# Performance work log

Measured on AMD Instinct MI355X. Metric: run time of the kernel, lower is better.

Reference implementation:

```python
import jax, jax.numpy as jnp
import numpy as np
from jax import lax

B, S, D, G, V = 32, 8, 128, 32, 64   # batch, slots, hidden_dim, grid_size, vocab_size
K, ED = 128, 32                       # VQ codebook size, code dim


def _conv(x, w, b, pad):
    # standard Conv2d, NCHW / OIHW
    y = lax.conv_general_dilated(x, w, (1, 1), [(pad, pad), (pad, pad)],
                                 dimension_numbers=('NCHW', 'OIHW', 'NCHW'))
    return y + b[None, :, None, None]


def _convT(x, w, b):
    # ConvTranspose2d(k=5, stride=1, padding=2) == conv with spatially flipped
    # kernel, padding k-1-p = 2, channels swapped (IOHW layout of torch weight).
    y = lax.conv_general_dilated(x, jnp.flip(w, (2, 3)), (1, 1), [(2, 2), (2, 2)],
                                 dimension_numbers=('NCHW', 'IOHW', 'NCHW'))
    return y + b[None, :, None, None]


def _build_grid(h, w):
    ys = jnp.linspace(0.0, 1.0, h)
    xs = jnp.linspace(0.0, 1.0, w)
    gy, gx = jnp.meshgrid(ys, xs, indexing='ij')
    g = jnp.stack([gy, gx], axis=-1)                 # [H,W,2]
    return jnp.concatenate([g, 1.0 - g], axis=-1)    # [H,W,4]


def setup_inputs() -> dict:
    key = jax.random.key(0)
    ks = jax.random.split(key, 20)
    sc = 0.05
    n = lambda k, sh: jax.random.normal(k, sh, jnp.float32) * sc
    return {
        'latent': jax.random.normal(ks[0], (B, S, D), jnp.float32),
        'pos_w': n(ks[1], (D, 4)),            # Linear(4, hidden): [out,in]
        'pos_b': jnp.zeros((D,), jnp.float32),
        'ct1_w': n(ks[2], (D, 64, 5, 5)),     # ConvTranspose2d: [in,out,kH,kW]
        'ct1_b': jnp.zeros((64,), jnp.float32),
        'ct2_w': n(ks[3], (64, 32, 5, 5)),
        'ct2_b': jnp.zeros((32,), jnp.float32),
        'codebook': jax.random.uniform(ks[4], (K, ED), jnp.float32, -1.0 / K, 1.0 / K),
        'c1_w': n(ks[5], (64, 32, 3, 3)),     # Conv2d: [out,in,kH,kW]
        'c1_b': jnp.zeros((64,), jnp.float32),
        'c2_w': n(ks[6], (V, 64, 3, 3)),
        'c2_b': jnp.zeros((V,), jnp.float32),
        'a1_w': n(ks[7], (64, 32, 3, 3)),
        'a1_b': jnp.zeros((64,), jnp.float32),
        'a2_w': n(ks[8], (1, 64, 3, 3)),
        'a2_b': jnp.zeros((1,), jnp.float32),
    }


def _forward(latent, pos_w, pos_b, ct1_w, ct1_b, ct2_w, ct2_b, codebook,
             c1_w, c1_b, c2_w, c2_b, a1_w, a1_b, a2_w, a2_b):
    b, s, d = latent.shape
    # spatial broadcast of slot latents -> [B*S, D, H, W]
    z = jnp.broadcast_to(latent.reshape(b * s, d, 1, 1), (b * s, d, G, G))
    # soft position embedding
    grid = _build_grid(G, G)                                  # [H,W,4]
    pos = (grid @ pos_w.T + pos_b).transpose(2, 0, 1)[None]   # [1,D,H,W]
    z = z + pos
    # ConvTranspose decoder
    h = jax.nn.relu(_convT(z, ct1_w, ct1_b))
    feat = jax.nn.relu(_convT(h, ct2_w, ct2_b))               # [B*S,32,H,W]
    # VQ bottleneck on channel-last features
    fp = feat.transpose(0, 2, 3, 1)                           # [B*S,H,W,32]
    flat = fp.reshape(-1, ED)                                 # [N,32]
    dist = (jnp.sum(flat * flat, axis=1, keepdims=True)
            + jnp.sum(codebook * codebook, axis=1)
            - 2.0 * flat @ codebook.T)                        # [N,K]
    idx = jnp.argmin(dist, axis=1)                            # [N]
    q = codebook[idx].reshape(fp.shape)                       # gather lookup
    e_loss = jnp.mean((lax.stop_gradient(q) - fp) ** 2)
    q_loss = jnp.mean((q - lax.stop_gradient(fp)) ** 2)
    vq_loss = q_loss + 0.25 * e_loss
    q_ste = fp + lax.stop_gradient(q - fp)                    # straight-through
    vq_feat = q_ste.transpose(0, 3, 1, 2)                     # [B*S,32,H,W]
    # heads
    colors = _conv(jax.nn.silu(_conv(vq_feat, c1_w, c1_b, 1)), c2_w, c2_b, 1)
    colors = colors.reshape(b, s, V, G, G)
    alphas = _conv(jax.nn.silu(_conv(feat, a1_w, a1_b, 1)), a2_w, a2_b, 1)
    alphas = alphas.reshape(b, s, 1, G, G)
    alphas_n = jax.nn.softmax(alphas, axis=1)
    recon = jnp.sum(alphas_n * colors, axis=1)                # [B,V,H,W]
    return recon, alphas_n, vq_loss


def reference(latent, pos_w, pos_b, ct1_w, ct1_b, ct2_w, ct2_b, codebook,
              c1_w, c1_b, c2_w, c2_b, a1_w, a1_b, a2_w, a2_b):
    return _forward(latent, pos_w, pos_b, ct1_w, ct1_b, ct2_w, ct2_b, codebook,
                    c1_w, c1_b, c2_w, c2_b, a1_w, a1_b, a2_w, a2_b)
```

## Files before the change

kernel.cpp:

```cpp
#include <hip/hip_runtime.h>
#include <math.h>

#define AOFF 2097152
#define LOFF 2359296

typedef __attribute__((ext_vector_type(8))) short short8;
typedef __attribute__((ext_vector_type(4))) float f32x4;

__device__ __forceinline__ int clsf(int v) { return v < 2 ? v : (v > 29 ? v - 27 : 2); }

__device__ __forceinline__ unsigned int f2bfu(float x) {
    unsigned int u = __float_as_uint(x);
    return (u + 0x7FFFu + ((u >> 16) & 1u)) >> 16;
}
__device__ __forceinline__ unsigned int cvt2(float a, float b) {
    return f2bfu(a) | (f2bfu(b) << 16);
}
__device__ __forceinline__ float bf2f(unsigned short u) {
    return __uint_as_float(((unsigned int)u) << 16);
}

__global__ void w1t_kernel(const float* __restrict__ w1, float* __restrict__ w1t) {
    int idx = blockIdx.x * 256 + threadIdx.x;
    if (idx >= 204800) return;
    int tap = idx % 25, rest = idx / 25;
    w1t[tap * 8192 + rest] = w1[idx];
}

__global__ void tapabc_kernel(const float* __restrict__ pw, const float* __restrict__ pb,
                              const float* __restrict__ w1t, float* __restrict__ tapabc) {
    __shared__ float A3[384];
    int tap = blockIdx.x, t = threadIdx.x;
    if (t < 128) {
        float p0 = pw[t * 4], p1 = pw[t * 4 + 1], p2 = pw[t * 4 + 2], p3 = pw[t * 4 + 3];
        A3[t] = p2 + p3 + pb[t];
        A3[128 + t] = p0 - p2;
        A3[256 + t] = p1 - p3;
    }
    __syncthreads();
    int o = t & 63, comp = t >> 6;
    const float* wp = w1t + tap * 8192 + o;
    const float* a = A3 + comp * 128;
    float s = 0.f;
    for (int i = 0; i < 128; ++i) s = fmaf(wp[i * 64], a[i], s);
    tapabc[(tap * 64 + o) * 3 + comp] = s;
}

__global__ void pfill_kernel(const float* __restrict__ tapabc, const float* __restrict__ b1,
                             float* __restrict__ P2) {
    __shared__ float uv[75];
    int o = blockIdx.x, t = threadIdx.x;
    if (t < 75) {
        int cls = t / 3, comp = t % 3;
        int cy = cls / 5, cx = cls % 5;
        const int klo[5] = {2, 1, 0, 0, 0}, khi[5] = {4, 4, 4, 3, 2};
        const float inv31 = 1.f / 31.f;
        float s = (comp == 0) ? b1[o] : 0.f;
        for (int ky = klo[cy]; ky <= khi[cy]; ++ky)
            for (int kx = klo[cx]; kx <= khi[cx]; ++kx) {
                int tap = (4 - ky) * 5 + (4 - kx);
                const float* tp = &tapabc[(tap * 64 + o) * 3];
                if (comp == 0) s += tp[0] + tp[1] * (ky - 2) * inv31 + tp[2] * (kx - 2) * inv31;
                else if (comp == 1) s += tp[1] * inv31;
                else s += tp[2] * inv31;
            }
        uv[t] = s;
    }
    __syncthreads();
    int y = t >> 5, x = t & 31;
    int cls = clsf(y) * 5 + clsf(x);
    float val = uv[cls * 3] + uv[cls * 3 + 1] * y + uv[cls * 3 + 2] * x;
    P2[((o >> 1) << 11) + (t << 1) + (o & 1)] = val;
}

__global__ void wsum_kernel(const float* __restrict__ w1, float* __restrict__ Wsum) {
    int idx = blockIdx.x * 256 + threadIdx.x;
    if (idx >= 25 * 128 * 64) return;
    int cls = idx >> 13;
    int i = (idx >> 6) & 127;
    int o = idx & 63;
    int cy = cls / 5, cx = cls % 5;
    const int klo[5] = {2, 1, 0, 0, 0}, khi[5] = {4, 4, 4, 3, 2};
    float s = 0.f;
    for (int ky = klo[cy]; ky <= khi[cy]; ++ky)
        for (int kx = klo[cx]; kx <= khi[cx]; ++kx)
            s += w1[(i * 64 + o) * 25 + (4 - ky) * 5 + (4 - kx)];
    Wsum[idx] = s;
}

__global__ void m_kernel(const float* __restrict__ latent, const float* __restrict__ Wsum,
                         float* __restrict__ M) {
    int n = blockIdx.x, cls = blockIdx.y, o = threadIdx.x;
    const float* l = &latent[n * 128];
    const float* w = &Wsum[cls * 8192 + o];
    float a0 = 0.f, a1 = 0.f;
    for (int i = 0; i < 128; i += 2) {
        a0 = fmaf(l[i], w[i * 64], a0);
        a1 = fmaf(l[i + 1], w[(i + 1) * 64], a1);
    }
    M[(n * 25 + cls) * 64 + o] = a0 + a1;
}

__global__ void prep_all_kernel(const float* __restrict__ a1w, const float* __restrict__ c1w,
                                const float* __restrict__ c2w, const float* __restrict__ ct2w,
                                short* __restrict__ wtall) {
    int gid = blockIdx.x * 256 + threadIdx.x;
    if (gid < 36864) {
        const float* src = gid < 18432 ? a1w : c1w;
        int idx = gid < 18432 ? gid : gid - 18432;
        int j = idx & 7, fi = idx >> 3;
        int o = fi % 64, g = (fi / 64) & 3, t = fi / 256;
        int i = g * 8 + j;
        wtall[gid] = (short)f2bfu(src[(o * 32 + i) * 9 + (t / 3) * 3 + (t % 3)]);
    } else if (gid < 73728) {
        int idx = gid - 36864;
        int j = idx & 7, fi = idx >> 3;
        int o = fi % 64, g = (fi / 64) & 3, ks = (fi / 256) & 1, t = fi / 512;
        int i = ks * 32 + g * 8 + j;
        wtall[gid] = (short)f2bfu(c2w[(o * 64 + i) * 9 + (t / 3) * 3 + (t % 3)]);
    } else if (gid < 124928) {
        int idx = gid - 73728;
        int j = idx & 7, fi = idx >> 3;
        int o = fi & 31, g = (fi >> 5) & 3, ks = (fi >> 7) & 1, t = fi >> 8;
        int i = ks * 32 + g * 8 + j;
        int ky = t / 5, kx = t % 5;
        wtall[gid] = (short)f2bfu(ct2w[((i * 32 + o) * 5 + (4 - ky)) * 5 + (4 - kx)]);
    }
}

__global__ __launch_bounds__(256, 4) void conv5_kernel(
        const float* __restrict__ M, const float* __restrict__ P2,
        const short* __restrict__ wt, const float* __restrict__ b2,
        unsigned short* __restrict__ featb) {
    __shared__ __align__(16) short tile[12 * 36 * 32];
    __shared__ float Ml[1600];
    const int n = blockIdx.x, y0 = blockIdx.y * 8;
    const int tid = threadIdx.x, w = tid >> 6, l = tid & 63;
    const int lx = l & 15, lg = l >> 4;

    for (int e = tid; e < 1600; e += 256) Ml[e] = M[n * 1600 + e];
    __syncthreads();

    f32x4 acc[2][2][2];
    #pragma unroll
    for (int m = 0; m < 2; ++m)
        #pragma unroll
        for (int q = 0; q < 2; ++q)
            #pragma unroll
            for (int c = 0; c < 2; ++c) acc[m][q][c] = (f32x4){0.f, 0.f, 0.f, 0.f};

    #pragma unroll 1
    for (int ks = 0; ks < 2; ++ks) {
        if (ks) __syncthreads();
        for (int e = tid; e < 6912; e += 256) {
            int cx = e % 36;
            int q = e / 36;
            int ipl = q & 15;
            int r = q >> 4;
            int gy = y0 - 2 + r, gx = cx - 2;
            unsigned int pack = 0u;
            if (gy >= 0 && gy < 32 && gx >= 0 && gx < 32) {
                int cls = clsf(gy) * 5 + clsf(gx);
                int pp = gy * 32 + gx;
                float2 pv = ((const float2*)P2)[((ks * 16 + ipl) << 10) + pp];
                float2 ml = ((const float2*)Ml)[cls * 32 + ks * 16 + ipl];
                pack = cvt2(fmaxf(ml.x + pv.x, 0.f), fmaxf(ml.y + pv.y, 0.f));
            }
            int off = ((r * 36 + cx) * 32 + 2 * ipl) * 2;
            off ^= (cx & 3) << 4;
            *(unsigned int*)((char*)tile + off) = pack;
        }
        __syncthreads();
        #pragma unroll 1
        for (int kx = 0; kx < 5; ++kx) {
            short8 af[5][2];
            #pragma unroll
            for (int ky = 0; ky < 5; ++ky)
                #pragma unroll
                for (int m = 0; m < 2; ++m)
                    af[ky][m] = *(const short8*)(wt + (ky * 5 + kx) * 2048 +
                                                 ((ks * 4 + lg) * 32 + m * 16 + lx) * 8);
            const int key = ((kx + lx) & 3) << 4;
            #pragma unroll
            for (int colf = 0; colf < 2; ++colf) {
                const int cbase = ((2 * w) * 36 + kx + colf * 16 + lx) * 64 + lg * 16;
                short8 bc[6];
                #pragma unroll
                for (int ir = 0; ir < 6; ++ir)
                    bc[ir] = *(const short8*)((char*)tile + ((cbase + ir * (36 * 64)) ^ key));
                #pragma unroll
                for (int ky = 0; ky < 5; ++ky)
                    #pragma unroll
                    for (int q = 0; q < 2; ++q)
                        #pragma unroll
                        for (int m = 0; m < 2; ++m)
                            acc[m][q][colf] = __builtin_amdgcn_mfma_f32_16x16x32_bf16(
                                af[ky][m], bc[q + ky], acc[m][q][colf], 0, 0, 0);
            }
        }
    }

    #pragma unroll
    for (int m = 0; m < 2; ++m)
        #pragma unroll
        for (int q = 0; q < 2; ++q)
            #pragma unroll
            for (int colf = 0; colf < 2; ++colf) {
                int yl = 2 * w + q, x = colf * 16 + lx;
                #pragma unroll
                for (int r = 0; r < 4; ++r) {
                    int och = m * 16 + lg * 4 + r;
                    float v = fmaxf(acc[m][q][colf][r] + b2[och], 0.f);
                    featb[(n * 32 + och) * 1024 + (y0 + yl) * 32 + x] = (unsigned short)f2bfu(v);
                }
            }
}

template<int I, int O, int ACT>
__global__ __launch_bounds__(256) void conv3_kernel(
        const unsigned short* __restrict__ in_, const short* __restrict__ wt,
        const float* __restrict__ bias, unsigned short* __restrict__ out_) {
    constexpr int KS = I / 32, MF = O / 16;
    constexpr int ABUF = KS * 4 * O * 8;
    __shared__ __align__(16) short smem[10 * 34 * 32];
    const int n = blockIdx.x, y0 = blockIdx.y * 8;
    const int tid = threadIdx.x, w = tid >> 6, l = tid & 63;
    const int lx = l & 15, lg = l >> 4;

    f32x4 acc[MF][2][2];
    #pragma unroll
    for (int m = 0; m < MF; ++m)
        #pragma unroll
        for (int q = 0; q < 2; ++q)
            #pragma unroll
            for (int c = 0; c < 2; ++c) acc[m][q][c] = (f32x4){0.f, 0.f, 0.f, 0.f};

    #pragma unroll 1
    for (int ks = 0; ks < KS; ++ks) {
        if (ks) __syncthreads();
        for (int e = tid; e < 5440; e += 256) {
            int cx = e % 34;
            int q = e / 34;
            int ip = q & 15;
            int r = q >> 4;
            int gy = y0 - 1 + r, gx = cx - 1;
            unsigned int pack = 0u;
            if (gy >= 0 && gy < 32 && gx >= 0 && gx < 32) {
                const unsigned short* p =
                    in_ + (n * I + ks * 32 + 2 * ip) * 1024 + gy * 32 + gx;
                pack = (unsigned int)p[0] | ((unsigned int)p[1024] << 16);
            }
            int off = ((r * 34 + cx) * 32 + 2 * ip) * 2;
            off ^= (cx & 7) << 4;
            *(unsigned int*)((char*)smem + off) = pack;
        }
        __syncthreads();
        #pragma unroll 1
        for (int kx = 0; kx < 3; ++kx) {
            short8 af[3][MF];
            #pragma unroll
            for (int ky = 0; ky < 3; ++ky)
                #pragma unroll
                for (int m = 0; m < MF; ++m)
                    af[ky][m] = *(const short8*)(wt + (ky * 3 + kx) * ABUF +
                                                 ((ks * 4 + lg) * O + m * 16 + lx) * 8);
            const int key = ((kx + lx) & 7) << 4;
            #pragma unroll
            for (int colf = 0; colf < 2; ++colf) {
                const int cbase = ((2 * w) * 34 + kx + colf * 16 + lx) * 64 + lg * 16;
                short8 bc[4];
                #pragma unroll
                for (int ir = 0; ir < 4; ++ir)
                    bc[ir] = *(const short8*)((char*)smem + ((cbase + ir * (34 * 64)) ^ key));
                #pragma unroll
                for (int ky = 0; ky < 3; ++ky)
                    #pragma unroll
                    for (int q = 0; q < 2; ++q)
                        #pragma unroll
                        for (int m = 0; m < MF; ++m)
                            acc[m][q][colf] = __builtin_amdgcn_mfma_f32_16x16x32_bf16(
                                af[ky][m], bc[q + ky], acc[m][q][colf], 0, 0, 0);
            }
        }
    }

    #pragma unroll
    for (int m = 0; m < MF; ++m)
        #pragma unroll
        for (int q = 0; q < 2; ++q)
            #pragma unroll
            for (int colf = 0; colf < 2; ++colf) {
                int yl = 2 * w + q, x = colf * 16 + lx;
                #pragma unroll
                for (int r = 0; r < 4; ++r) {
                    int och = m * 16 + lg * 4 + r;
                    float v = acc[m][q][colf][r] + bias[och];
                    if (ACT == 1) v = v / (1.f + expf(-v));
                    out_[(n * O + och) * 1024 + (y0 + yl) * 32 + x] = (unsigned short)f2bfu(v);
                }
            }
}

__global__ void a2dot_kernel(const unsigned short* __restrict__ in, const float* __restrict__ w,
                             float* __restrict__ s9) {
    __shared__ float wl[576];
    int t = threadIdx.x;
    for (int e = t; e < 576; e += 256) wl[e] = w[e];
    __syncthreads();
    int p = blockIdx.x * 256 + t;
    int n = p >> 10, yx = p & 1023;
    float acc[9];
    #pragma unroll
    for (int k = 0; k < 9; ++k) acc[k] = 0.f;
    const unsigned short* ip = in + n * 65536 + yx;
    for (int i = 0; i < 64; ++i) {
        float v = bf2f(ip[i * 1024]);
        #pragma unroll
        for (int k = 0; k < 9; ++k) acc[k] = fmaf(v, wl[i * 9 + k], acc[k]);
    }
    #pragma unroll
    for (int k = 0; k < 9; ++k) s9[(k << 18) + p] = acc[k];
}

__global__ void a2soft_kernel(const float* __restrict__ s9, const float* __restrict__ b2,
                              float* __restrict__ outp) {
    int idx = blockIdx.x * 256 + threadIdx.x;
    if (idx >= 32 * 1024) return;
    int bb = idx >> 10, yx = idx & 1023;
    int y = yx >> 5, x = yx & 31;
    float v[8];
    float bias = b2[0];
    #pragma unroll
    for (int s = 0; s < 8; ++s) {
        int n = bb * 8 + s;
        float a = bias;
        #pragma unroll
        for (int ky = 0; ky < 3; ++ky) {
            int yy = y + ky - 1;
            if (yy < 0 || yy > 31) continue;
            #pragma unroll
            for (int kx = 0; kx < 3; ++kx) {
                int xx = x + kx - 1;
                if (xx < 0 || xx > 31) continue;
                a += s9[((ky * 3 + kx) << 18) + (n << 10) + yy * 32 + xx];
            }
        }
        v[s] = a;
    }
    float m = -3.4e38f;
    #pragma unroll
    for (int s = 0; s < 8; ++s) m = fmaxf(m, v[s]);
    float sum = 0.f;
    #pragma unroll
    for (int s = 0; s < 8; ++s) { v[s] = expf(v[s] - m); sum += v[s]; }
    float inv = 1.f / sum;
    #pragma unroll
    for (int s = 0; s < 8; ++s) outp[AOFF + ((bb * 8 + s) << 10) + yx] = v[s] * inv;
}

__global__ __launch_bounds__(256) void vq_mfma_kernel(
        const unsigned short* __restrict__ featb, const float* __restrict__ codebook,
        unsigned short* __restrict__ qfeat, float* __restrict__ partial) {
    __shared__ float cbf[4096];
    __shared__ __align__(16) short cbh[4096];
    __shared__ float cn[128];
    __shared__ float red[4];
    const int tid = threadIdx.x;
    const int w = tid >> 6, l = tid & 63;
    const int lx = l & 15, lg = l >> 4;

    for (int e = tid; e < 4096; e += 256) {
        float v = codebook[e];
        cbf[e] = v;
        int code = e >> 5, d = e & 31;
        int off = (code * 32 + d) * 2;
        off ^= (code & 7) << 4;
        *(short*)((char*)cbh + off) = (short)f2bfu(v);
    }
    __syncthreads();
    if (tid < 128) {
        float s = 0.f;
        #pragma unroll
        for (int c = 0; c < 32; ++c) { float v = cbf[tid * 32 + c]; s = fmaf(v, v, s); }
        cn[tid] = s;
    }
    short8 af[8];
    #pragma unroll
    for (int m = 0; m < 8; ++m) {
        int code = m * 16 + lx;
        int off = (code * 32 + lg * 8) * 2;
        off ^= (code & 7) << 4;
        af[m] = *(const short8*)((char*)cbh + off);
    }
    __syncthreads();
    float cnh[8][4];
    #pragma unroll
    for (int m = 0; m < 8; ++m)
        #pragma unroll
        for (int r = 0; r < 4; ++r)
            cnh[m][r] = 0.5f * cn[m * 16 + lg * 4 + r];

    const int n = blockIdx.x >> 2;
    const int yxw = (blockIdx.x & 3) * 256 + w * 64;
    const unsigned short* fb = featb + n * 32768;
    float lloss = 0.f;

    #pragma unroll 1
    for (int pxg = 0; pxg < 4; ++pxg) {
        int yx = yxw + pxg * 16 + lx;
        const unsigned short* fp = fb + (lg * 8) * 1024 + yx;
        union { short8 s; unsigned int u[4]; } bb;
        #pragma unroll
        for (int k = 0; k < 4; ++k)
            bb.u[k] = (unsigned int)fp[(2 * k) * 1024] | ((unsigned int)fp[(2 * k + 1) * 1024] << 16);
        f32x4 S[8];
        #pragma unroll
        for (int m = 0; m < 8; ++m)
            S[m] = __builtin_amdgcn_mfma_f32_16x16x32_bf16(
                af[m], bb.s, (f32x4){0.f, 0.f, 0.f, 0.f}, 0, 0, 0);
        float bestv = -3.4e38f; int besti = 0;
        #pragma unroll
        for (int m = 0; m < 8; ++m)
            #pragma unroll
            for (int r = 0; r < 4; ++r) {
                float v = S[m][r] - cnh[m][r];
                int code = m * 16 + lg * 4 + r;
                if (v > bestv) { bestv = v; besti = code; }
            }
        #pragma unroll
        for (int d = 16; d < 64; d <<= 1) {
            float ov = __shfl_xor(bestv, d);
            int oi = __shfl_xor(besti, d);
            if (ov > bestv || (ov == bestv && oi < besti)) { bestv = ov; besti = oi; }
        }
        int offq = (besti * 32 + lg * 8) * 2;
        offq ^= (besti & 7) << 4;
        short8 qh = *(const short8*)((char*)cbh + offq);
        unsigned short* qp = qfeat + (n * 32 + lg * 8) * 1024 + yx;
        const float* qf = &cbf[besti * 32 + lg * 8];
        #pragma unroll
        for (int j = 0; j < 8; ++j) {
            qp[j * 1024] = (unsigned short)qh[j];
            float fv = bf2f((unsigned short)bb.s[j]);
            float dd = qf[j] - fv;
            lloss = fmaf(dd, dd, lloss);
        }
    }
    for (int off = 32; off > 0; off >>= 1) lloss += __shfl_down(lloss, off);
    if (l == 0) red[w] = lloss;
    __syncthreads();
    if (tid == 0) partial[blockIdx.x] = (red[0] + red[1]) + (red[2] + red[3]);
}

__global__ void recon_kernel(const unsigned short* __restrict__ colors, float* __restrict__ outp) {
    int idx = blockIdx.x * 256 + threadIdx.x;
    int yx = idx & 1023;
    int v = (idx >> 10) & 63;
    int bb = idx >> 16;
    float acc = 0.f;
    #pragma unroll
    for (int s = 0; s < 8; ++s) {
        float a = outp[AOFF + ((bb * 8 + s) << 10) + yx];
        float c = bf2f(colors[((bb * 8 + s) * 64 + v) * 1024 + yx]);
        acc = fmaf(a, c, acc);
    }
    outp[idx] = acc;
}

__global__ void loss_kernel(const float* __restrict__ partial, float* __restrict__ outp) {
    __shared__ float red[4];
    int t = threadIdx.x;
    float s = 0.f;
    for (int i = t; i < 1024; i += 256) s += partial[i];
    for (int o = 32; o > 0; o >>= 1) s += __shfl_down(s, o);
    if ((t & 63) == 0) red[t >> 6] = s;
    __syncthreads();
    if (t == 0) outp[LOFF] = 1.25f * ((red[0] + red[1]) + (red[2] + red[3])) / 8388608.0f;
}

extern "C" void kernel_launch(void* const* d_in, const int* in_sizes, int n_in,
                              void* d_out, int out_size, void* d_ws, size_t ws_size,
                              hipStream_t stream) {
    const float* latent  = (const float*)d_in[0];
    const float* pos_w   = (const float*)d_in[1];
    const float* pos_b   = (const float*)d_in[2];
    const float* ct1_w   = (const float*)d_in[3];
    const float* ct1_b   = (const float*)d_in[4];
    const float* ct2_w   = (const float*)d_in[5];
    const float* ct2_b   = (const float*)d_in[6];
    const float* codebook= (const float*)d_in[7];
    const float* c1_w    = (const float*)d_in[8];
    const float* c1_b    = (const float*)d_in[9];
    const float* c2_w    = (const float*)d_in[10];
    const float* c2_b    = (const float*)d_in[11];
    const float* a1_w    = (const float*)d_in[12];
    const float* a1_b    = (const float*)d_in[13];
    const float* a2_w    = (const float*)d_in[14];
    const float* a2_b    = (const float*)d_in[15];
    float* out = (float*)d_out;

    float* ws     = (float*)d_ws;
    unsigned short* featb = (unsigned short*)ws;
    float* s9     = ws + 8388608;
    float* tapabc = s9 + 2359296;
    float* P      = tapabc + 4800;
    float* M      = P + 65536;
    float* partial= M + 409600;
    float* w1t    = partial + 1024;
    float* Wsum   = w1t + 204800;
    short* wtall  = (short*)(Wsum + 204800);
    short* wtA    = wtall;
    short* wtC1   = wtall + 18432;
    short* wtC2   = wtall + 36864;
    short* wtT2   = wtall + 73728;
    unsigned short* tmpb    = (unsigned short*)(wtall + 124928);
    unsigned short* qfeatb  = tmpb + 16777216;
    unsigned short* colorsb = qfeatb + 8388608;

    w1t_kernel<<<800, 256, 0, stream>>>(ct1_w, w1t);
    tapabc_kernel<<<25, 192, 0, stream>>>(pos_w, pos_b, w1t, tapabc);
    pfill_kernel<<<64, 1024, 0, stream>>>(tapabc, ct1_b, P);
    wsum_kernel<<<800, 256, 0, stream>>>(ct1_w, Wsum);
    m_kernel<<<dim3(256, 25), 64, 0, stream>>>(latent, Wsum, M);
    prep_all_kernel<<<488, 256, 0, stream>>>(a1_w, c1_w, c2_w, ct2_w, wtall);

    conv5_kernel<<<dim3(256, 4), 256, 0, stream>>>(M, P, wtT2, ct2_b, featb);
    conv3_kernel<32, 64, 1><<<dim3(256, 4), 256, 0, stream>>>(featb, wtA, a1_b, tmpb);
    a2dot_kernel<<<1024, 256, 0, stream>>>(tmpb, a2_w, s9);
    a2soft_kernel<<<128, 256, 0, stream>>>(s9, a2_b, out);
    vq_mfma_kernel<<<1024, 256, 0, stream>>>(featb, codebook, qfeatb, partial);
    conv3_kernel<32, 64, 1><<<dim3(256, 4), 256, 0, stream>>>(qfeatb, wtC1, c1_b, tmpb);
    conv3_kernel<64, 64, 0><<<dim3(256, 4), 256, 0, stream>>>(tmpb, wtC2, c2_b, colorsb);
    recon_kernel<<<8192, 256, 0, stream>>>(colorsb, out);
    loss_kernel<<<1, 256, 0, stream>>>(partial, out);
}
```

Measured before the change: 261.4 us.

## Fuse VQ lookup with a1 and c1 convolutions; prefetch c2 input into registers

A new kernel loads each feature tile into LDS once and runs the VQ argmin over the halo tile, writing quantized codes straight into a second LDS tile. It then runs both the alpha-head a1 conv and the color-head c1 conv from LDS, so the qfeat buffer is no longer written to and re-read from global memory, and two launches are removed. The VQ work is repeated for halo pixels, and the LDS footprint grows, which may reduce occupancy. The c2 conv now loads its second input-channel slab into registers while the first slab is being computed, overlapping global loads with MFMA work.

```diff
diff --git a/kernel.cpp b/kernel.cpp
--- a/kernel.cpp
+++ b/kernel.cpp
@@ -216,76 +216,269 @@
             }
 }
 
-template<int I, int O, int ACT>
-__global__ __launch_bounds__(256) void conv3_kernel(
+__device__ __forceinline__ void conv3x3_silu_lds(
+        const short* __restrict__ tile, const short* __restrict__ wt,
+        const float* __restrict__ bias, unsigned short* __restrict__ outp,
+        int n, int y0, int w, int lx, int lg) {
+    f32x4 acc[4][2][2];
+    #pragma unroll
+    for (int m = 0; m < 4; ++m)
+        #pragma unroll
+        for (int q = 0; q < 2; ++q)
+            #pragma unroll
+            for (int c = 0; c < 2; ++c) acc[m][q][c] = (f32x4){0.f, 0.f, 0.f, 0.f};
+    #pragma unroll 1
+    for (int kx = 0; kx < 3; ++kx) {
+        short8 af3[3][4];
+        #pragma unroll
+        for (int ky = 0; ky < 3; ++ky)
+            #pragma unroll
+            for (int m = 0; m < 4; ++m)
+                af3[ky][m] = *(const short8*)(wt + (ky * 3 + kx) * 2048 +
+                                              (lg * 64 + m * 16 + lx) * 8);
+        const int key = ((kx + lx) & 7) << 4;
+        #pragma unroll
+        for (int colf = 0; colf < 2; ++colf) {
+            const int cbase = ((2 * w) * 34 + kx + colf * 16 + lx) * 64 + lg * 16;
+            short8 bc[4];
+            #pragma unroll
+            for (int ir = 0; ir < 4; ++ir)
+                bc[ir] = *(const short8*)((const char*)tile + ((cbase + ir * (34 * 64)) ^ key));
+            #pragma unroll
+            for (int ky = 0; ky < 3; ++ky)
+                #pragma unroll
+                for (int q = 0; q < 2; ++q)
+                    #pragma unroll
+                    for (int m = 0; m < 4; ++m)
+                        acc[m][q][colf] = __builtin_amdgcn_mfma_f32_16x16x32_bf16(
+                            af3[ky][m], bc[q + ky], acc[m][q][colf], 0, 0, 0);
+        }
+    }
+    #pragma unroll
+    for (int m = 0; m < 4; ++m)
+        #pragma unroll
+        for (int q = 0; q < 2; ++q)
+            #pragma unroll
+            for (int colf = 0; colf < 2; ++colf) {
+                int yl = 2 * w + q, x = colf * 16 + lx;
+                #pragma unroll
+                for (int r = 0; r < 4; ++r) {
+                    int och = m * 16 + lg * 4 + r;
+                    float v = acc[m][q][colf][r] + bias[och];
+                    v = v / (1.f + expf(-v));
+                    outp[(n * 64 + och) * 1024 + (y0 + yl) * 32 + x] = (unsigned short)f2bfu(v);
+                }
+            }
+}
+
+__global__ __launch_bounds__(256) void vqhead_kernel(
+        const unsigned short* __restrict__ featb, const float* __restrict__ codebook,
+        const short* __restrict__ wtA, const float* __restrict__ a1b,
+        const short* __restrict__ wtC1, const float* __restrict__ c1b,
+        unsigned short* __restrict__ a1out, unsigned short* __restrict__ c1out,
+        float* __restrict__ partial) {
+    __shared__ __align__(16) short ftile[10 * 34 * 32];
+    __shared__ __align__(16) short qtile[10 * 34 * 32];
+    __shared__ __align__(16) short cbh[4096];
+    __shared__ float cn[128];
+    __shared__ float red[4];
+    const int n = blockIdx.x, y0 = blockIdx.y * 8;
+    const int tid = threadIdx.x, w = tid >> 6, l = tid & 63;
+    const int lx = l & 15, lg = l >> 4;
+
+    for (int e = tid; e < 4096; e += 256) {
+        int code = e >> 5, d = e & 31;
+        int off = (code * 32 + d) * 2;
+        off ^= (code & 7) << 4;
+        *(short*)((char*)cbh + off) = (short)f2bfu(codebook[e]);
+    }
+    if (tid < 128) {
+        float s = 0.f;
+        #pragma unroll
+        for (int c = 0; c < 32; ++c) { float v = codebook[tid * 32 + c]; s = fmaf(v, v, s); }
+        cn[tid] = s;
+    }
+    for (int e = tid; e < 5440; e += 256) {
+        int cx = e % 34;
+        int q = e / 34;
+        int ip = q & 15;
+        int r = q >> 4;
+        int gy = y0 - 1 + r, gx = cx - 1;
+        unsigned int pack = 0u;
+        if (gy >= 0 && gy < 32 && gx >= 0 && gx < 32) {
+            const unsigned short* p = featb + (n * 32 + 2 * ip) * 1024 + gy * 32 + gx;
+            pack = (unsigned int)p[0] | ((unsigned int)p[1024] << 16);
+        }
+        int off = ((r * 34 + cx) * 32 + 2 * ip) * 2;
+        off ^= (cx & 7) << 4;
+        *(unsigned int*)((char*)ftile + off) = pack;
+    }
+    __syncthreads();
+
+    short8 af[8];
+    #pragma unroll
+    for (int m = 0; m < 8; ++m) {
+        int off = ((m * 16 + lx) * 32 + lg * 8) * 2;
+        off ^= (lx & 7) << 4;
+        af[m] = *(const short8*)((char*)cbh + off);
+    }
+    float cnh[8][4];
+    #pragma unroll
+    for (int m = 0; m < 8; ++m)
+        #pragma unroll
+        for (int r = 0; r < 4; ++r)
+            cnh[m][r] = 0.5f * cn[m * 16 + lg * 4 + r];
+
+    float lloss = 0.f;
+    int g0 = w * 6;
+    int g1 = g0 + 6 > 22 ? 22 : g0 + 6;
+    #pragma unroll 1
+    for (int g = g0; g < g1; ++g) {
+        int px = g * 16 + lx;
+        bool valid = px < 340;
+        int r = px / 34, cx = px - r * 34;
+        int gy = y0 - 1 + r, gx = cx - 1;
+        bool inimg = valid && gy >= 0 && gy < 32 && gx >= 0 && gx < 32;
+        short8 bbs = (short8){0, 0, 0, 0, 0, 0, 0, 0};
+        int baddr = (px * 64 + lg * 16) ^ ((cx & 7) << 4);
+        if (valid) bbs = *(const short8*)((const char*)ftile + baddr);
+        f32x4 S[8];
+        #pragma unroll
+        for (int m = 0; m < 8; ++m)
+            S[m] = __builtin_amdgcn_mfma_f32_16x16x32_bf16(
+                af[m], bbs, (f32x4){0.f, 0.f, 0.f, 0.f}, 0, 0, 0);
+        float bestv = -3.4e38f; int besti = 0;
+        #pragma unroll
+        for (int m = 0; m < 8; ++m)
+            #pragma unroll
+            for (int r4 = 0; r4 < 4; ++r4) {
+                float v = S[m][r4] - cnh[m][r4];
+                int code = m * 16 + lg * 4 + r4;
+                if (v > bestv) { bestv = v; besti = code; }
+            }
+        #pragma unroll
+        for (int d = 16; d < 64; d <<= 1) {
+            float ov = __shfl_xor(bestv, d);
+            int oi = __shfl_xor(besti, d);
+            if (ov > bestv || (ov == bestv && oi < besti)) { bestv = ov; besti = oi; }
+        }
+        if (inimg) {
+            int offq = (besti * 32 + lg * 8) * 2;
+            offq ^= (besti & 7) << 4;
+            short8 qh = *(const short8*)((char*)cbh + offq);
+            *(short8*)((char*)qtile + baddr) = qh;
+            if (r >= 1 && r <= 8 && cx >= 1 && cx <= 32) {
+                #pragma unroll
+                for (int j = 0; j < 8; ++j) {
+                    float dd = bf2f((unsigned short)qh[j]) - bf2f((unsigned short)bbs[j]);
+                    lloss = fmaf(dd, dd, lloss);
+                }
+            }
+        } else if (valid) {
+            *(short8*)((char*)qtile + baddr) = (short8){0, 0, 0, 0, 0, 0, 0, 0};
+        }
+    }
+    for (int off = 32; off > 0; off >>= 1) lloss += __shfl_down(lloss, off);
+    if (l == 0) red[w] = lloss;
+
+    conv3x3_silu_lds(ftile, wtA, a1b, a1out, n, y0, w, lx, lg);
+
+    __syncthreads();
+
+    conv3x3_silu_lds(qtile, wtC1, c1b, c1out, n, y0, w, lx, lg);
+
+    if (tid == 0)
+        partial[blockIdx.y * 256 + blockIdx.x] = (red[0] + red[1]) + (red[2] + red[3]);
+}
+
+__global__ __launch_bounds__(256) void c2_kernel(
         const unsigned short* __restrict__ in_, const short* __restrict__ wt,
         const float* __restrict__ bias, unsigned short* __restrict__ out_) {
-    constexpr int KS = I / 32, MF = O / 16;
-    constexpr int ABUF = KS * 4 * O * 8;
     __shared__ __align__(16) short smem[10 * 34 * 32];
     const int n = blockIdx.x, y0 = blockIdx.y * 8;
     const int tid = threadIdx.x, w = tid >> 6, l = tid & 63;
     const int lx = l & 15, lg = l >> 4;
 
-    f32x4 acc[MF][2][2];
-    #pragma unroll
-    for (int m = 0; m < MF; ++m)
+    f32x4 acc[4][2][2];
+    #pragma unroll
+    for (int m = 0; m < 4; ++m)
         #pragma unroll
         for (int q = 0; q < 2; ++q)
             #pragma unroll
             for (int c = 0; c < 2; ++c) acc[m][q][c] = (f32x4){0.f, 0.f, 0.f, 0.f};
 
-    #pragma unroll 1
-    for (int ks = 0; ks < KS; ++ks) {
-        if (ks) __syncthreads();
-        for (int e = tid; e < 5440; e += 256) {
-            int cx = e % 34;
-            int q = e / 34;
-            int ip = q & 15;
-            int r = q >> 4;
-            int gy = y0 - 1 + r, gx = cx - 1;
-            unsigned int pack = 0u;
-            if (gy >= 0 && gy < 32 && gx >= 0 && gx < 32) {
-                const unsigned short* p =
-                    in_ + (n * I + ks * 32 + 2 * ip) * 1024 + gy * 32 + gx;
-                pack = (unsigned int)p[0] | ((unsigned int)p[1024] << 16);
-            }
-            int off = ((r * 34 + cx) * 32 + 2 * ip) * 2;
-            off ^= (cx & 7) << 4;
-            *(unsigned int*)((char*)smem + off) = pack;
-        }
-        __syncthreads();
-        #pragma unroll 1
-        for (int kx = 0; kx < 3; ++kx) {
-            short8 af[3][MF];
-            #pragma unroll
-            for (int ky = 0; ky < 3; ++ky)
-                #pragma unroll
-                for (int m = 0; m < MF; ++m)
-                    af[ky][m] = *(const short8*)(wt + (ky * 3 + kx) * ABUF +
-                                                 ((ks * 4 + lg) * O + m * 16 + lx) * 8);
-            const int key = ((kx + lx) & 7) << 4;
-            #pragma unroll
-            for (int colf = 0; colf < 2; ++colf) {
-                const int cbase = ((2 * w) * 34 + kx + colf * 16 + lx) * 64 + lg * 16;
-                short8 bc[4];
-                #pragma unroll
-                for (int ir = 0; ir < 4; ++ir)
-                    bc[ir] = *(const short8*)((char*)smem + ((cbase + ir * (34 * 64)) ^ key));
-                #pragma unroll
-                for (int ky = 0; ky < 3; ++ky)
-                    #pragma unroll
-                    for (int q = 0; q < 2; ++q)
-                        #pragma unroll
-                        for (int m = 0; m < MF; ++m)
-                            acc[m][q][colf] = __builtin_amdgcn_mfma_f32_16x16x32_bf16(
-                                af[ky][m], bc[q + ky], acc[m][q][colf], 0, 0, 0);
-            }
-        }
-    }
-
-    #pragma unroll
-    for (int m = 0; m < MF; ++m)
+    unsigned int rg[22];
+
+#define C2_LOAD(KSV)                                                         \
+    _Pragma("unroll")                                                        \
+    for (int it = 0; it < 22; ++it) {                                        \
+        int e = tid + it * 256;                                              \
+        unsigned int pack = 0u;                                              \
+        if (e < 5440) {                                                      \
+            int cx = e % 34; int q = e / 34; int ip = q & 15; int r = q >> 4;\
+            int gy = y0 - 1 + r, gx = cx - 1;                                \
+            if (gy >= 0 && gy < 32 && gx >= 0 && gx < 32) {                  \
+                const unsigned short* p =                                    \
+                    in_ + (n * 64 + (KSV) * 32 + 2 * ip) * 1024 + gy * 32 + gx; \
+                pack = (unsigned int)p[0] | ((unsigned int)p[1024] << 16);   \
+            }                                                                \
+        }                                                                    \
+        rg[it] = pack;                                                       \
+    }
+
+#define C2_WRITE()                                                           \
+    _Pragma("unroll")                                                        \
+    for (int it = 0; it < 22; ++it) {                                        \
+        int e = tid + it * 256;                                              \
+        if (e < 5440) {                                                      \
+            int cx = e % 34; int q = e / 34; int ip = q & 15; int r = q >> 4;\
+            int off = ((r * 34 + cx) * 32 + 2 * ip) * 2;                     \
+            off ^= (cx & 7) << 4;                                            \
+            *(unsigned int*)((char*)smem + off) = rg[it];                    \
+        }                                                                    \
+    }
+
+#define C2_COMPUTE(KSV)                                                      \
+    _Pragma("unroll 1")                                                      \
+    for (int kx = 0; kx < 3; ++kx) {                                         \
+        short8 af3[3][4];                                                    \
+        _Pragma("unroll")                                                    \
+        for (int ky = 0; ky < 3; ++ky)                                       \
+            _Pragma("unroll")                                                \
+            for (int m = 0; m < 4; ++m)                                      \
+                af3[ky][m] = *(const short8*)(wt + (ky * 3 + kx) * 4096 +    \
+                                ((KSV * 4 + lg) * 64 + m * 16 + lx) * 8);    \
+        const int key = ((kx + lx) & 7) << 4;                                \
+        _Pragma("unroll")                                                    \
+        for (int colf = 0; colf < 2; ++colf) {                               \
+            const int cbase = ((2 * w) * 34 + kx + colf * 16 + lx) * 64 + lg * 16; \
+            short8 bc[4];                                                    \
+            _Pragma("unroll")                                                \
+            for (int ir = 0; ir < 4; ++ir)                                   \
+                bc[ir] = *(const short8*)((char*)smem + ((cbase + ir * (34 * 64)) ^ key)); \
+            _Pragma("unroll")                                                \
+            for (int ky = 0; ky < 3; ++ky)                                   \
+                _Pragma("unroll")                                            \
+                for (int q = 0; q < 2; ++q)                                  \
+                    _Pragma("unroll")                                        \
+                    for (int m = 0; m < 4; ++m)                              \
+                        acc[m][q][colf] = __builtin_amdgcn_mfma_f32_16x16x32_bf16( \
+                            af3[ky][m], bc[q + ky], acc[m][q][colf], 0, 0, 0); \
+        }                                                                    \
+    }
+
+    C2_LOAD(0)
+    C2_WRITE()
+    C2_LOAD(1)
+    __syncthreads();
+    C2_COMPUTE(0)
+    __syncthreads();
+    C2_WRITE()
+    __syncthreads();
+    C2_COMPUTE(1)
+
+    #pragma unroll
+    for (int m = 0; m < 4; ++m)
         #pragma unroll
         for (int q = 0; q < 2; ++q)
             #pragma unroll
@@ -295,8 +488,7 @@
                 for (int r = 0; r < 4; ++r) {
                     int och = m * 16 + lg * 4 + r;
                     float v = acc[m][q][colf][r] + bias[och];
-                    if (ACT == 1) v = v / (1.f + expf(-v));
-                    out_[(n * O + och) * 1024 + (y0 + yl) * 32 + x] = (unsigned short)f2bfu(v);
+                    out_[(n * 64 + och) * 1024 + (y0 + yl) * 32 + x] = (unsigned short)f2bfu(v);
                 }
             }
 }
@@ -356,100 +548,6 @@
     float inv = 1.f / sum;
     #pragma unroll
     for (int s = 0; s < 8; ++s) outp[AOFF + ((bb * 8 + s) << 10) + yx] = v[s] * inv;
-}
-
-__global__ __launch_bounds__(256) void vq_mfma_kernel(
-        const unsigned short* __restrict__ featb, const float* __restrict__ codebook,
-        unsigned short* __restrict__ qfeat, float* __restrict__ partial) {
-    __shared__ float cbf[4096];
-    __shared__ __align__(16) short cbh[4096];
-    __shared__ float cn[128];
-    __shared__ float red[4];
-    const int tid = threadIdx.x;
-    const int w = tid >> 6, l = tid & 63;
-    const int lx = l & 15, lg = l >> 4;
-
-    for (int e = tid; e < 4096; e += 256) {
-        float v = codebook[e];
-        cbf[e] = v;
-        int code = e >> 5, d = e & 31;
-        int off = (code * 32 + d) * 2;
-        off ^= (code & 7) << 4;
-        *(short*)((char*)cbh + off) = (short)f2bfu(v);
-    }
-    __syncthreads();
-    if (tid < 128) {
-        float s = 0.f;
-        #pragma unroll
-        for (int c = 0; c < 32; ++c) { float v = cbf[tid * 32 + c]; s = fmaf(v, v, s); }
-        cn[tid] = s;
-    }
-    short8 af[8];
-    #pragma unroll
-    for (int m = 0; m < 8; ++m) {
-        int code = m * 16 + lx;
-        int off = (code * 32 + lg * 8) * 2;
-        off ^= (code & 7) << 4;
-        af[m] = *(const short8*)((char*)cbh + off);
-    }
-    __syncthreads();
-    float cnh[8][4];
-    #pragma unroll
-    for (int m = 0; m < 8; ++m)
-        #pragma unroll
-        for (int r = 0; r < 4; ++r)
-            cnh[m][r] = 0.5f * cn[m * 16 + lg * 4 + r];
-
-    const int n = blockIdx.x >> 2;
-    const int yxw = (blockIdx.x & 3) * 256 + w * 64;
-    const unsigned short* fb = featb + n * 32768;
-    float lloss = 0.f;
-
-    #pragma unroll 1
-    for (int pxg = 0; pxg < 4; ++pxg) {
-        int yx = yxw + pxg * 16 + lx;
-        const unsigned short* fp = fb + (lg * 8) * 1024 + yx;
-        union { short8 s; unsigned int u[4]; } bb;
-        #pragma unroll
-        for (int k = 0; k < 4; ++k)
-            bb.u[k] = (unsigned int)fp[(2 * k) * 1024] | ((unsigned int)fp[(2 * k + 1) * 1024] << 16);
-        f32x4 S[8];
-        #pragma unroll
-        for (int m = 0; m < 8; ++m)
-            S[m] = __builtin_amdgcn_mfma_f32_16x16x32_bf16(
-                af[m], bb.s, (f32x4){0.f, 0.f, 0.f, 0.f}, 0, 0, 0);
-        float bestv = -3.4e38f; int besti = 0;
-        #pragma unroll
-        for (int m = 0; m < 8; ++m)
-            #pragma unroll
-            for (int r = 0; r < 4; ++r) {
-                float v = S[m][r] - cnh[m][r];
-                int code = m * 16 + lg * 4 + r;
-                if (v > bestv) { bestv = v; besti = code; }
-            }
-        #pragma unroll
-        for (int d = 16; d < 64; d <<= 1) {
-            float ov = __shfl_xor(bestv, d);
-            int oi = __shfl_xor(besti, d);
-            if (ov > bestv || (ov == bestv && oi < besti)) { bestv = ov; besti = oi; }
-        }
-        int offq = (besti * 32 + lg * 8) * 2;
-        offq ^= (besti & 7) << 4;
-        short8 qh = *(const short8*)((char*)cbh + offq);
-        unsigned short* qp = qfeat + (n * 32 + lg * 8) * 1024 + yx;
-        const float* qf = &cbf[besti * 32 + lg * 8];
-        #pragma unroll
-        for (int j = 0; j < 8; ++j) {
-            qp[j * 1024] = (unsigned short)qh[j];
-            float fv = bf2f((unsigned short)bb.s[j]);
-            float dd = qf[j] - fv;
-            lloss = fmaf(dd, dd, lloss);
-        }
-    }
-    for (int off = 32; off > 0; off >>= 1) lloss += __shfl_down(lloss, off);
-    if (l == 0) red[w] = lloss;
-    __syncthreads();
-    if (tid == 0) partial[blockIdx.x] = (red[0] + red[1]) + (red[2] + red[3]);
 }
 
 __global__ void recon_kernel(const unsigned short* __restrict__ colors, float* __restrict__ outp) {
@@ -514,8 +612,8 @@
     short* wtC2   = wtall + 36864;
     short* wtT2   = wtall + 73728;
     unsigned short* tmpb    = (unsigned short*)(wtall + 124928);
-    unsigned short* qfeatb  = tmpb + 16777216;
-    unsigned short* colorsb = qfeatb + 8388608;
+    unsigned short* c1out   = tmpb + 16777216;
+    unsigned short* colorsb = c1out + 16777216;
 
     w1t_kernel<<<800, 256, 0, stream>>>(ct1_w, w1t);
     tapabc_kernel<<<25, 192, 0, stream>>>(pos_w, pos_b, w1t, tapabc);
@@ -525,12 +623,11 @@
     prep_all_kernel<<<488, 256, 0, stream>>>(a1_w, c1_w, c2_w, ct2_w, wtall);
 
     conv5_kernel<<<dim3(256, 4), 256, 0, stream>>>(M, P, wtT2, ct2_b, featb);
-    conv3_kernel<32, 64, 1><<<dim3(256, 4), 256, 0, stream>>>(featb, wtA, a1_b, tmpb);
+    vqhead_kernel<<<dim3(256, 4), 256, 0, stream>>>(
+        featb, codebook, wtA, a1_b, wtC1, c1_b, tmpb, c1out, partial);
     a2dot_kernel<<<1024, 256, 0, stream>>>(tmpb, a2_w, s9);
     a2soft_kernel<<<128, 256, 0, stream>>>(s9, a2_b, out);
-    vq_mfma_kernel<<<1024, 256, 0, stream>>>(featb, codebook, qfeatb, partial);
-    conv3_kernel<32, 64, 1><<<dim3(256, 4), 256, 0, stream>>>(qfeatb, wtC1, c1_b, tmpb);
-    conv3_kernel<64, 64, 0><<<dim3(256, 4), 256, 0, stream>>>(tmpb, wtC2, c2_b, colorsb);
+    c2_kernel<<<dim3(256, 4), 256, 0, stream>>>(c1out, wtC2, c2_b, colorsb);
     recon_kernel<<<8192, 256, 0, stream>>>(colorsb, out);
     loss_kernel<<<1, 256, 0, stream>>>(partial, out);
 }
```

Result: slower. 280.8 us (+7.4%).

## Switch intermediate bf16 activations from channel-major to pixel-major layout

Applied to the files above, without the earlier changes.

Intermediate feature maps (featb, tmpb, qfeat, colors) are now stored with channels innermost per pixel, NHWC-style, instead of channel-planar. Conv epilogues pack four bf16 outputs into one 64-bit store, and the conv3 smem fill, vq, a2dot and recon kernels read with 16-byte vector loads. This replaces many strided 2-byte global accesses with contiguous wide ones. The recon kernel is restructured so each thread accumulates 32 vocab channels, which raises register use and reduces parallelism to 256 blocks.

```diff
diff --git a/kernel.cpp b/kernel.cpp
--- a/kernel.cpp
+++ b/kernel.cpp
@@ -207,12 +207,15 @@
             #pragma unroll
             for (int colf = 0; colf < 2; ++colf) {
                 int yl = 2 * w + q, x = colf * 16 + lx;
+                unsigned long long pk = 0ull;
                 #pragma unroll
                 for (int r = 0; r < 4; ++r) {
                     int och = m * 16 + lg * 4 + r;
                     float v = fmaxf(acc[m][q][colf][r] + b2[och], 0.f);
-                    featb[(n * 32 + och) * 1024 + (y0 + yl) * 32 + x] = (unsigned short)f2bfu(v);
+                    pk |= (unsigned long long)f2bfu(v) << (16 * r);
                 }
+                *(unsigned long long*)(featb + (n * 1024 + (y0 + yl) * 32 + x) * 32
+                                       + m * 16 + lg * 4) = pk;
             }
 }
 
@@ -238,21 +241,16 @@
     #pragma unroll 1
     for (int ks = 0; ks < KS; ++ks) {
         if (ks) __syncthreads();
-        for (int e = tid; e < 5440; e += 256) {
-            int cx = e % 34;
-            int q = e / 34;
-            int ip = q & 15;
-            int r = q >> 4;
+        for (int e = tid; e < 1360; e += 256) {
+            int px = e >> 2, qc = e & 3;
+            int r = px / 34, cx = px - r * 34;
             int gy = y0 - 1 + r, gx = cx - 1;
-            unsigned int pack = 0u;
-            if (gy >= 0 && gy < 32 && gx >= 0 && gx < 32) {
-                const unsigned short* p =
-                    in_ + (n * I + ks * 32 + 2 * ip) * 1024 + gy * 32 + gx;
-                pack = (unsigned int)p[0] | ((unsigned int)p[1024] << 16);
-            }
-            int off = ((r * 34 + cx) * 32 + 2 * ip) * 2;
+            short8 v8 = (short8){0, 0, 0, 0, 0, 0, 0, 0};
+            if (gy >= 0 && gy < 32 && gx >= 0 && gx < 32)
+                v8 = *(const short8*)(in_ + (n * 1024 + gy * 32 + gx) * I + ks * 32 + qc * 8);
+            int off = (px * 32 + qc * 8) * 2;
             off ^= (cx & 7) << 4;
-            *(unsigned int*)((char*)smem + off) = pack;
+            *(short8*)((char*)smem + off) = v8;
         }
         __syncthreads();
         #pragma unroll 1
@@ -291,13 +289,16 @@
             #pragma unroll
             for (int colf = 0; colf < 2; ++colf) {
                 int yl = 2 * w + q, x = colf * 16 + lx;
+                unsigned long long pk = 0ull;
                 #pragma unroll
                 for (int r = 0; r < 4; ++r) {
                     int och = m * 16 + lg * 4 + r;
                     float v = acc[m][q][colf][r] + bias[och];
                     if (ACT == 1) v = v / (1.f + expf(-v));
-                    out_[(n * O + och) * 1024 + (y0 + yl) * 32 + x] = (unsigned short)f2bfu(v);
+                    pk |= (unsigned long long)f2bfu(v) << (16 * r);
                 }
+                *(unsigned long long*)(out_ + (n * 1024 + (y0 + yl) * 32 + x) * O
+                                       + m * 16 + lg * 4) = pk;
             }
 }
 
@@ -308,15 +309,19 @@
     for (int e = t; e < 576; e += 256) wl[e] = w[e];
     __syncthreads();
     int p = blockIdx.x * 256 + t;
-    int n = p >> 10, yx = p & 1023;
     float acc[9];
     #pragma unroll
     for (int k = 0; k < 9; ++k) acc[k] = 0.f;
-    const unsigned short* ip = in + n * 65536 + yx;
-    for (int i = 0; i < 64; ++i) {
-        float v = bf2f(ip[i * 1024]);
-        #pragma unroll
-        for (int k = 0; k < 9; ++k) acc[k] = fmaf(v, wl[i * 9 + k], acc[k]);
+    const unsigned short* ip = in + (long long)p * 64;
+    #pragma unroll
+    for (int c8 = 0; c8 < 8; ++c8) {
+        short8 v8 = *(const short8*)(ip + c8 * 8);
+        #pragma unroll
+        for (int j = 0; j < 8; ++j) {
+            float v = bf2f((unsigned short)v8[j]);
+            #pragma unroll
+            for (int k = 0; k < 9; ++k) acc[k] = fmaf(v, wl[(c8 * 8 + j) * 9 + k], acc[k]);
+        }
     }
     #pragma unroll
     for (int k = 0; k < 9; ++k) s9[(k << 18) + p] = acc[k];
@@ -402,22 +407,17 @@
 
     const int n = blockIdx.x >> 2;
     const int yxw = (blockIdx.x & 3) * 256 + w * 64;
-    const unsigned short* fb = featb + n * 32768;
     float lloss = 0.f;
 
     #pragma unroll 1
     for (int pxg = 0; pxg < 4; ++pxg) {
         int yx = yxw + pxg * 16 + lx;
-        const unsigned short* fp = fb + (lg * 8) * 1024 + yx;
-        union { short8 s; unsigned int u[4]; } bb;
-        #pragma unroll
-        for (int k = 0; k < 4; ++k)
-            bb.u[k] = (unsigned int)fp[(2 * k) * 1024] | ((unsigned int)fp[(2 * k + 1) * 1024] << 16);
+        short8 bbs = *(const short8*)(featb + (n * 1024 + yx) * 32 + lg * 8);
         f32x4 S[8];
         #pragma unroll
         for (int m = 0; m < 8; ++m)
             S[m] = __builtin_amdgcn_mfma_f32_16x16x32_bf16(
-                af[m], bb.s, (f32x4){0.f, 0.f, 0.f, 0.f}, 0, 0, 0);
+                af[m], bbs, (f32x4){0.f, 0.f, 0.f, 0.f}, 0, 0, 0);
         float bestv = -3.4e38f; int besti = 0;
         #pragma unroll
         for (int m = 0; m < 8; ++m)
@@ -436,12 +436,11 @@
         int offq = (besti * 32 + lg * 8) * 2;
         offq ^= (besti & 7) << 4;
         short8 qh = *(const short8*)((char*)cbh + offq);
-        unsigned short* qp = qfeat + (n * 32 + lg * 8) * 1024 + yx;
+        *(short8*)(qfeat + (n * 1024 + yx) * 32 + lg * 8) = qh;
         const float* qf = &cbf[besti * 32 + lg * 8];
         #pragma unroll
         for (int j = 0; j < 8; ++j) {
-            qp[j * 1024] = (unsigned short)qh[j];
-            float fv = bf2f((unsigned short)bb.s[j]);
+            float fv = bf2f((unsigned short)bbs[j]);
             float dd = qf[j] - fv;
             lloss = fmaf(dd, dd, lloss);
         }
@@ -452,19 +451,30 @@
     if (tid == 0) partial[blockIdx.x] = (red[0] + red[1]) + (red[2] + red[3]);
 }
 
-__global__ void recon_kernel(const unsigned short* __restrict__ colors, float* __restrict__ outp) {
-    int idx = blockIdx.x * 256 + threadIdx.x;
-    int yx = idx & 1023;
-    int v = (idx >> 10) & 63;
-    int bb = idx >> 16;
-    float acc = 0.f;
-    #pragma unroll
+__global__ __launch_bounds__(256) void recon_kernel(
+        const unsigned short* __restrict__ colors, float* __restrict__ outp) {
+    const int b = blockIdx.x, y8 = blockIdx.y;
+    const int tid = threadIdx.x;
+    const int yxl = tid & 127, vh = tid >> 7;
+    const int yx = y8 * 128 + yxl;
+    float acc[32];
+    #pragma unroll
+    for (int v = 0; v < 32; ++v) acc[v] = 0.f;
+    #pragma unroll 1
     for (int s = 0; s < 8; ++s) {
-        float a = outp[AOFF + ((bb * 8 + s) << 10) + yx];
-        float c = bf2f(colors[((bb * 8 + s) * 64 + v) * 1024 + yx]);
-        acc = fmaf(a, c, acc);
-    }
-    outp[idx] = acc;
+        float a = outp[AOFF + ((b * 8 + s) << 10) + yx];
+        const unsigned short* cp = colors + ((b * 8 + s) * 1024 + yx) * 64 + vh * 32;
+        #pragma unroll
+        for (int k = 0; k < 4; ++k) {
+            short8 v8 = *(const short8*)(cp + k * 8);
+            #pragma unroll
+            for (int j = 0; j < 8; ++j)
+                acc[k * 8 + j] = fmaf(a, bf2f((unsigned short)v8[j]), acc[k * 8 + j]);
+        }
+    }
+    #pragma unroll
+    for (int v = 0; v < 32; ++v)
+        outp[(b * 64 + vh * 32 + v) * 1024 + yx] = acc[v];
 }
 
 __global__ void loss_kernel(const float* __restrict__ partial, float* __restrict__ outp) {
@@ -531,6 +541,6 @@
     vq_mfma_kernel<<<1024, 256, 0, stream>>>(featb, codebook, qfeatb, partial);
     conv3_kernel<32, 64, 1><<<dim3(256, 4), 256, 0, stream>>>(qfeatb, wtC1, c1_b, tmpb);
     conv3_kernel<64, 64, 0><<<dim3(256, 4), 256, 0, stream>>>(tmpb, wtC2, c2_b, colorsb);
-    recon_kernel<<<8192, 256, 0, stream>>>(colorsb, out);
+    recon_kernel<<<dim3(32, 8), 256, 0, stream>>>(colorsb, out);
     loss_kernel<<<1, 256, 0, stream>>>(partial, out);
 }
```

Measured after the change: 230.5 us. -11.8%, faster.
